# Kernel tuning notes

Measured on AMD Instinct MI355X. Metric: run time of the kernel, lower is better.

Reference implementation:

```python
import jax, jax.numpy as jnp
import numpy as np

N = 50000   # nodes
E = 800000  # edges
IN, H, O, C = 128, 256, 256, 64
G = 64      # graphs in batch


def setup_inputs() -> dict:
    key = jax.random.key(0)
    ks = jax.random.split(key, 10)
    x = jax.random.normal(ks[0], (N, IN), dtype=jnp.float32)
    edge_index = jax.random.randint(ks[1], (2, E), 0, N, dtype=jnp.int32)
    batch = jnp.sort(jax.random.randint(ks[2], (N,), 0, G, dtype=jnp.int32))
    # learned params (PyG GCNConv: weight [in, out] + bias [out]; nn.Linear)
    W1 = jax.random.normal(ks[3], (IN, H), dtype=jnp.float32) / np.sqrt(IN)
    b1 = jnp.zeros((H,), dtype=jnp.float32)
    W2 = jax.random.normal(ks[4], (H, O), dtype=jnp.float32) / np.sqrt(H)
    b2 = jnp.zeros((O,), dtype=jnp.float32)
    Wfc = jax.random.normal(ks[5], (O, C), dtype=jnp.float32) / np.sqrt(O)
    bfc = jnp.zeros((C,), dtype=jnp.float32)
    return {"x": x, "edge_index": edge_index, "batch": batch,
            "W1": W1, "b1": b1, "W2": W2, "b2": b2, "Wfc": Wfc, "bfc": bfc}


def reference(x, edge_index, batch, W1, b1, W2, b2, Wfc, bfc):
    src, dst = edge_index[0], edge_index[1]
    # degree with self-loops (PyG GCNConv default: add_self_loops=True, sym norm)
    deg = jax.ops.segment_sum(jnp.ones((E,), x.dtype), dst, num_segments=N) + 1.0
    dinv = jax.lax.rsqrt(deg)                      # D^{-1/2}
    edge_norm = (dinv[src] * dinv[dst])[:, None]   # [E, 1]
    self_norm = (dinv * dinv)[:, None]             # [N, 1] self-loop weight

    def gcn_conv(h, W, b):
        h = h @ W                                  # transform first (PyG order)
        agg = jax.ops.segment_sum(h[src] * edge_norm, dst, num_segments=N)
        return agg + h * self_norm + b

    h = jax.nn.gelu(gcn_conv(x, W1, b1), approximate=False)  # nn.GELU exact
    h = gcn_conv(h, W2, b2)

    # global_mean_pool over graph ids
    cnt = jax.ops.segment_sum(jnp.ones((N,), h.dtype), batch, num_segments=G)
    pooled = jax.ops.segment_sum(h, batch, num_segments=G) / jnp.maximum(cnt, 1.0)[:, None]
    return pooled @ Wfc + bfc                      # [G, C]
```

## Files before the change

kernel.cpp:

```cpp
#include <hip/hip_runtime.h>
#include <hip/hip_bf16.h>
#include <hip/hip_fp16.h>
#include <math.h>

#define NNODES 50000
#define NEDGES 800000
#define FIN 128
#define FH 256
#define NG 64
#define NC 64
#define NP 50176
#define QSK 196
#define SPLITX_ITEMS (NNODES * FIN / 4)
#define SPLITX_BLOCKS ((SPLITX_ITEMS + 255) / 256)
#define W1T_BLOCKS (FIN * 256 / 256)
#define GEMM_MB ((NNODES + 127) / 128)
#define GEMM_BLKS (GEMM_MB * 2)
#define QTR (NP / 4)

#define NBUCK 196
#define BCAP 5120
#define BIN_CHUNK 2048
#define BIN_BLOCKS ((NEDGES + BIN_CHUNK - 1) / BIN_CHUNK)

typedef unsigned short bhalf;
typedef __attribute__((ext_vector_type(8))) short bf16x8;
typedef __attribute__((ext_vector_type(4))) float f32x4;
typedef __attribute__((ext_vector_type(4))) unsigned short u16x4;

__device__ inline bhalf f2bf_rn(float f) {
    unsigned int u = __float_as_uint(f);
    u += 0x7FFFu + ((u >> 16) & 1u);
    return (bhalf)(u >> 16);
}
__device__ inline float bf2f(bhalf h) { return __uint_as_float(((unsigned int)h) << 16); }
__device__ inline float2 bfpair(unsigned int u) {
    return make_float2(__uint_as_float(u << 16), __uint_as_float(u & 0xFFFF0000u));
}


__global__ void splitx_kernel(const float* __restrict__ x, bhalf* __restrict__ xb,
                              const float* __restrict__ W1, bhalf* __restrict__ w1t,
                              int* __restrict__ bcur) {
    int b = blockIdx.x;
    if (b < SPLITX_BLOCKS) {
        int i = b * 256 + threadIdx.x;
        if (i < SPLITX_ITEMS) {
            float4 v = *reinterpret_cast<const float4*>(&x[i * 4]);
            u16x4 o = {f2bf_rn(v.x), f2bf_rn(v.y), f2bf_rn(v.z), f2bf_rn(v.w)};
            *reinterpret_cast<u16x4*>(&xb[i * 4]) = o;
        }
    } else if (b < SPLITX_BLOCKS + W1T_BLOCKS) {
        int i = (b - SPLITX_BLOCKS) * 256 + threadIdx.x;
        int k = i >> 8, n = i & 255;
        w1t[n * FIN + k] = f2bf_rn(W1[i]);
    } else {
        if (threadIdx.x < NBUCK) bcur[threadIdx.x] = threadIdx.x * BCAP;
    }
}


__global__ __launch_bounds__(256)
void bin_kernel(const int* __restrict__ src, const int* __restrict__ dst,
                int* __restrict__ bcur, unsigned int* __restrict__ binned) {
    __shared__ int hist[NBUCK];
    __shared__ int base[NBUCK];
    __shared__ int gb[NBUCK];
    __shared__ int lcur[NBUCK];
    __shared__ int scan_tmp[256];
    __shared__ unsigned int stage[BIN_CHUNK];
    __shared__ unsigned char bid[BIN_CHUNK];
    int t = threadIdx.x;
    int e0 = blockIdx.x * BIN_CHUNK;
    for (int i = t; i < NBUCK; i += 256) hist[i] = 0;
    __syncthreads();
#pragma unroll
    for (int k = 0; k < BIN_CHUNK / 256; k++) {
        int e = e0 + k * 256 + t;
        if (e < NEDGES) atomicAdd(&hist[dst[e] >> 8], 1);
    }
    __syncthreads();
    int v = (t < NBUCK) ? hist[t] : 0;
    scan_tmp[t] = v;
    __syncthreads();
#pragma unroll
    for (int off = 1; off < 256; off <<= 1) {
        int x = (t >= off) ? scan_tmp[t - off] : 0;
        __syncthreads();
        scan_tmp[t] += x;
        __syncthreads();
    }
    if (t < NBUCK) {
        int ex = scan_tmp[t] - v;
        base[t] = ex;
        lcur[t] = ex;
        gb[t] = (v > 0) ? atomicAdd(&bcur[t], v) : 0;
    }
    __syncthreads();
#pragma unroll
    for (int k = 0; k < BIN_CHUNK / 256; k++) {
        int e = e0 + k * 256 + t;
        if (e < NEDGES) {
            int s = src[e], d = dst[e];
            int b = d >> 8;
            int lp = atomicAdd(&lcur[b], 1);
            stage[lp] = (unsigned int)s | ((unsigned int)(d & 255) << 16);
            bid[lp] = (unsigned char)b;
        }
    }
    __syncthreads();
    int total = base[NBUCK - 1] + hist[NBUCK - 1];
    for (int i = t; i < total; i += 256) {
        int b = bid[i];
        binned[(size_t)gb[b] + (i - base[b])] = stage[i];
    }
}


__global__ __launch_bounds__(256)
void place_kernel(const unsigned int* __restrict__ binned, const int* __restrict__ bcur,
                  int* __restrict__ row_start, float* __restrict__ dinv,
                  unsigned int* __restrict__ edata) {
    __shared__ unsigned int stage[BCAP];
    __shared__ int sc[256];
    __shared__ int deg[256];
    __shared__ int lex[256];
    __shared__ int lcur[256];
    __shared__ unsigned short dih[256];
    __shared__ int s_ebase, s_cnt;
    int b = blockIdx.x, t = threadIdx.x;
    int c = (t < NBUCK) ? (bcur[t] - t * BCAP) : 0;
    sc[t] = c;
    __syncthreads();
#pragma unroll
    for (int off = 1; off < 256; off <<= 1) {
        int x = (t >= off) ? sc[t - off] : 0;
        __syncthreads();
        sc[t] += x;
        __syncthreads();
    }
    if (t == b) { s_ebase = sc[t] - c; s_cnt = c; }
    deg[t] = 0;
    __syncthreads();
    int cnt = s_cnt, eb = s_ebase;
    const unsigned int* bp = &binned[(size_t)b * BCAP];
    for (int i = t; i < cnt; i += 256) stage[i] = bp[i];
    __syncthreads();
    for (int i = t; i < cnt; i += 256) atomicAdd(&deg[(stage[i] >> 16) & 255], 1);
    __syncthreads();
    int d = deg[t];
    float di = rsqrtf((float)d + 1.0f);
    int gn = (b << 8) + t;
    if (gn < NNODES) dinv[gn] = di;
    dih[t] = __half_as_ushort(__float2half(di));
    sc[t] = d;
    __syncthreads();
#pragma unroll
    for (int off = 1; off < 256; off <<= 1) {
        int x = (t >= off) ? sc[t - off] : 0;
        __syncthreads();
        sc[t] += x;
        __syncthreads();
    }
    int lexv = sc[t] - d;
    lex[t] = lexv;
    lcur[t] = 0;
    if (gn <= NNODES) row_start[gn] = eb + lexv;
    __syncthreads();
    for (int i = t; i < cnt; i += 256) {
        unsigned int e = stage[i];
        int dl = (e >> 16) & 255;
        int pos = eb + lex[dl] + atomicAdd(&lcur[dl], 1);
        edata[pos] = (e & 0xFFFFu) | ((unsigned int)dih[dl] << 16);
    }
}


__global__ __launch_bounds__(256)
void gather128_kernel(const bhalf* __restrict__ xb, const unsigned int* __restrict__ edata,
                      const int* __restrict__ row_start, const float* __restrict__ dinv,
                      bhalf* __restrict__ z, int Nn) {
    int node = blockIdx.x * 4 + (threadIdx.x >> 6);
    if (node >= Nn) return;
    int lane = threadIdx.x & 63;
    int st = row_start[node];
    int cnt = row_start[node + 1] - st;
    float ax = 0.0f, ay = 0.0f;
    int j = 0;
    for (; j + 3 < cnt; j += 4) {
        unsigned int e0 = edata[st + j],     e1 = edata[st + j + 1];
        unsigned int e2 = edata[st + j + 2], e3 = edata[st + j + 3];
        int s0 = e0 & 0xFFFFu, s1 = e1 & 0xFFFFu, s2 = e2 & 0xFFFFu, s3 = e3 & 0xFFFFu;
        float2 v0 = bfpair(*reinterpret_cast<const unsigned int*>(&xb[(size_t)s0 * FIN + lane * 2]));
        float2 v1 = bfpair(*reinterpret_cast<const unsigned int*>(&xb[(size_t)s1 * FIN + lane * 2]));
        float2 v2 = bfpair(*reinterpret_cast<const unsigned int*>(&xb[(size_t)s2 * FIN + lane * 2]));
        float2 v3 = bfpair(*reinterpret_cast<const unsigned int*>(&xb[(size_t)s3 * FIN + lane * 2]));
        float n0 = dinv[s0], n1 = dinv[s1], n2 = dinv[s2], n3 = dinv[s3];
        ax += v0.x * n0 + v1.x * n1 + v2.x * n2 + v3.x * n3;
        ay += v0.y * n0 + v1.y * n1 + v2.y * n2 + v3.y * n3;
    }
    for (; j < cnt; j++) {
        unsigned int e0 = edata[st + j];
        int s0 = e0 & 0xFFFFu;
        float2 v0 = bfpair(*reinterpret_cast<const unsigned int*>(&xb[(size_t)s0 * FIN + lane * 2]));
        float n0 = dinv[s0];
        ax += v0.x * n0; ay += v0.y * n0;
    }
    float dn = dinv[node];
    float2 xv = bfpair(*reinterpret_cast<const unsigned int*>(&xb[(size_t)node * FIN + lane * 2]));
    ushort2 o = {f2bf_rn(dn * (ax + xv.x * dn)), f2bf_rn(dn * (ay + xv.y * dn))};
    *reinterpret_cast<ushort2*>(&z[(size_t)node * FIN + lane * 2]) = o;
}


__global__ __launch_bounds__(256)
void wt_build_kernel(const unsigned int* __restrict__ edata, const int* __restrict__ row_start,
                     const int* __restrict__ batch, const float* __restrict__ dinv,
                     bhalf* __restrict__ wthi, bhalf* __restrict__ wtlo) {
    __shared__ float acc[QTR];
    int g = blockIdx.x >> 2;
    int q = blockIdx.x & 3;
    int base = q * QTR;
    for (int i = threadIdx.x; i < QTR; i += 256) acc[i] = 0.0f;
    int lo = 0, hi = NNODES;
    while (lo < hi) { int m = (lo + hi) >> 1; if (batch[m] < g) lo = m + 1; else hi = m; }
    int na = lo;
    hi = NNODES;
    while (lo < hi) { int m = (lo + hi) >> 1; if (batch[m] < g + 1) lo = m + 1; else hi = m; }
    int nb = lo;
    int pa = row_start[na];
    int pb = row_start[nb];
    __syncthreads();
    for (int p = pa + threadIdx.x; p < pb; p += 256) {
        unsigned int e = edata[p];
        int s = (int)(e & 0xFFFFu) - base;
        if ((unsigned int)s < (unsigned int)QTR)
            atomicAdd(&acc[s], __half2float(__ushort_as_half((unsigned short)(e >> 16))));
    }
    __syncthreads();
    size_t rowo = (size_t)g * NP + base;
    for (int i = threadIdx.x; i < QTR; i += 256) {
        int s = base + i;
        float dv = (s < NNODES) ? dinv[s] : 0.0f;
        float v = acc[i];
        if (s >= na && s < nb) v += dv;
        v *= dv;
        bhalf hb = f2bf_rn(v);
        wthi[rowo + i] = hb;
        wtlo[rowo + i] = f2bf_rn(v - bf2f(hb));
    }
}


__global__ __launch_bounds__(256)
void gemm_kernel(const bhalf* __restrict__ A, const bhalf* __restrict__ Bt,
                 const float* __restrict__ bias, bhalf* __restrict__ h1t, int M, int Kp) {
    __shared__ bhalf As[128 * 72];
    __shared__ bhalf Bs[128 * 72];
    const int tid  = threadIdx.x;
    const int lane = tid & 63;
    const int wave = tid >> 6;
    const int quad = lane >> 4;
    const int l15  = lane & 15;
    const int wm = (wave & 1) * 64;
    const int wn = (wave >> 1) * 64;
    const int bm = (blockIdx.x >> 1) * 128;
    const int bn = (blockIdx.x & 1) * 128;

    f32x4 acc[4][4] = {};

    for (int k0 = 0; k0 < Kp; k0 += 64) {
#pragma unroll
        for (int i = 0; i < 4; i++) {
            int chunk = tid + i * 256;
            int r = chunk >> 3, c16 = chunk & 7;
            int gm = bm + r;
            float4 va = make_float4(0.f, 0.f, 0.f, 0.f);
            if (gm < M) va = *reinterpret_cast<const float4*>(&A[(size_t)gm * Kp + k0 + c16 * 8]);
            *reinterpret_cast<float4*>(&As[r * 72 + c16 * 8]) = va;
            float4 vb = *reinterpret_cast<const float4*>(&Bt[(size_t)(bn + r) * Kp + k0 + c16 * 8]);
            *reinterpret_cast<float4*>(&Bs[r * 72 + c16 * 8]) = vb;
        }
        __syncthreads();
#pragma unroll
        for (int kk = 0; kk < 64; kk += 32) {
            bf16x8 af[4], bfr[4];
#pragma unroll
            for (int mi = 0; mi < 4; mi++)
                af[mi] = *reinterpret_cast<const bf16x8*>(&As[(wm + mi * 16 + l15) * 72 + kk + quad * 8]);
#pragma unroll
            for (int ni = 0; ni < 4; ni++)
                bfr[ni] = *reinterpret_cast<const bf16x8*>(&Bs[(wn + ni * 16 + l15) * 72 + kk + quad * 8]);
#pragma unroll
            for (int mi = 0; mi < 4; mi++)
#pragma unroll
                for (int ni = 0; ni < 4; ni++)
                    acc[mi][ni] = __builtin_amdgcn_mfma_f32_16x16x32_bf16(af[mi], bfr[ni], acc[mi][ni], 0, 0, 0);
        }
        __syncthreads();
    }

#pragma unroll
    for (int mi = 0; mi < 4; mi++) {
        int row0 = bm + wm + mi * 16 + quad * 4;
#pragma unroll
        for (int ni = 0; ni < 4; ni++) {
            int col = bn + wn + ni * 16 + l15;
            float bv = bias[col];
            u16x4 o;
#pragma unroll
            for (int r = 0; r < 4; r++) {
                float v = acc[mi][ni][r] + bv;
                v = 0.5f * v * (1.0f + erff(v * 0.70710678118654752f));
                o[r] = f2bf_rn(v);
            }
            *reinterpret_cast<u16x4*>(&h1t[(size_t)col * NP + row0]) = o;
        }
    }
}


__global__ __launch_bounds__(256)
void qsum_mfma_kernel(const bhalf* __restrict__ h1t, const bhalf* __restrict__ wthi,
                      const bhalf* __restrict__ wtlo, float* __restrict__ qpart) {
    const int tid  = threadIdx.x;
    const int lane = tid & 63;
    const int wave = tid >> 6;
    const int quad = lane >> 4;
    const int l15  = lane & 15;
    const int m0 = wave * 64;
    const size_t kbase = (size_t)blockIdx.x * 256 + quad * 8;
    f32x4 acc[4][4] = {};
#pragma unroll
    for (int ks = 0; ks < 8; ks++) {
        size_t k0 = kbase + ks * 32;
        bf16x8 af[4], bh[4], bl[4];
#pragma unroll
        for (int mi = 0; mi < 4; mi++)
            af[mi] = *reinterpret_cast<const bf16x8*>(&h1t[(size_t)(m0 + mi * 16 + l15) * NP + k0]);
#pragma unroll
        for (int ni = 0; ni < 4; ni++) {
            bh[ni] = *reinterpret_cast<const bf16x8*>(&wthi[(size_t)(ni * 16 + l15) * NP + k0]);
            bl[ni] = *reinterpret_cast<const bf16x8*>(&wtlo[(size_t)(ni * 16 + l15) * NP + k0]);
        }
#pragma unroll
        for (int mi = 0; mi < 4; mi++)
#pragma unroll
            for (int ni = 0; ni < 4; ni++) {
                acc[mi][ni] = __builtin_amdgcn_mfma_f32_16x16x32_bf16(af[mi], bh[ni], acc[mi][ni], 0, 0, 0);
                acc[mi][ni] = __builtin_amdgcn_mfma_f32_16x16x32_bf16(af[mi], bl[ni], acc[mi][ni], 0, 0, 0);
            }
    }
    float* qp = &qpart[(size_t)blockIdx.x * NG * FH];
#pragma unroll
    for (int mi = 0; mi < 4; mi++) {
        int row0 = m0 + mi * 16 + quad * 4;
#pragma unroll
        for (int ni = 0; ni < 4; ni++) {
            int col = ni * 16 + l15;
            f32x4 o = {acc[mi][ni][0], acc[mi][ni][1], acc[mi][ni][2], acc[mi][ni][3]};
            *reinterpret_cast<f32x4*>(&qp[(size_t)col * FH + row0]) = o;
        }
    }
}


__global__ __launch_bounds__(256)
void p2fc_kernel(const float* __restrict__ qpart, const float* __restrict__ W2,
                 const float* __restrict__ b2, const int* __restrict__ batch,
                 const float* __restrict__ Wfc, const float* __restrict__ bfc,
                 float* __restrict__ out) {
    __shared__ float qg[FH];
    __shared__ float ps[FH];
    int g = blockIdx.x;
    int t = threadIdx.x;
    float s = 0.0f;
    for (int b = 0; b < QSK; b++)
        s += qpart[(size_t)b * NG * FH + (size_t)g * FH + t];
    qg[t] = s;
    int lo = 0, hi = NNODES;
    while (lo < hi) { int m = (lo + hi) >> 1; if (batch[m] < g) lo = m + 1; else hi = m; }
    int a = lo;
    lo = 0; hi = NNODES;
    while (lo < hi) { int m = (lo + hi) >> 1; if (batch[m] < g + 1) lo = m + 1; else hi = m; }
    float inv = 1.0f / fmaxf((float)(lo - a), 1.0f);
    __syncthreads();
    float acc = 0.0f;
    for (int k = 0; k < FH; k++)
        acc += qg[k] * W2[k * FH + t];
    ps[t] = acc * inv + b2[t];
    __syncthreads();
    if (t < NC) {
        float a2 = 0.0f;
        for (int cc = 0; cc < FH; cc++)
            a2 += ps[cc] * Wfc[cc * NC + t];
        out[g * NC + t] = a2 + bfc[t];
    }
}


extern "C" void kernel_launch(void* const* d_in, const int* in_sizes, int n_in,
                              void* d_out, int out_size, void* d_ws, size_t ws_size,
                              hipStream_t stream) {
    const float* x    = (const float*)d_in[0];
    const int*   ei   = (const int*)d_in[1];
    const int*   batch= (const int*)d_in[2];
    const float* W1   = (const float*)d_in[3];
    const float* b1   = (const float*)d_in[4];
    const float* W2   = (const float*)d_in[5];
    const float* b2   = (const float*)d_in[6];
    const float* Wfc  = (const float*)d_in[7];
    const float* bfc  = (const float*)d_in[8];
    float* out = (float*)d_out;

    const int* src = ei;
    const int* dst = ei + NEDGES;

    bhalf* xb        = (bhalf*)d_ws;
    bhalf* zb        = xb + (size_t)NNODES * FIN;
    bhalf* h1t       = zb + (size_t)NNODES * FIN;
    unsigned int* edata  = (unsigned int*)(h1t + (size_t)FH * NP);
    unsigned int* binned = edata + NEDGES;
    int*   row_start = (int*)(binned + (size_t)NBUCK * BCAP);
    int*   bcur      = row_start + NNODES + 256;
    float* dinv      = (float*)(bcur + 256);
    bhalf* w1t       = (bhalf*)(dinv + NNODES + 256);
    bhalf* wthi      = w1t + 256 * FIN;
    bhalf* wtlo      = wthi + (size_t)NG * NP;
    float* qpart     = (float*)(wtlo + (size_t)NG * NP);

    splitx_kernel<<<SPLITX_BLOCKS + W1T_BLOCKS + 1, 256, 0, stream>>>(x, xb, W1, w1t, bcur);
    bin_kernel<<<BIN_BLOCKS, 256, 0, stream>>>(src, dst, bcur, binned);
    place_kernel<<<NBUCK, 256, 0, stream>>>(binned, bcur, row_start, dinv, edata);

    gather128_kernel<<<(NNODES + 3) / 4, 256, 0, stream>>>(xb, edata, row_start, dinv,
                                                           zb, NNODES);
    wt_build_kernel<<<NG * 4, 256, 0, stream>>>(edata, row_start, batch, dinv, wthi, wtlo);
    gemm_kernel<<<GEMM_BLKS, 256, 0, stream>>>(zb, w1t, b1, h1t, NNODES, FIN);

    qsum_mfma_kernel<<<QSK, 256, 0, stream>>>(h1t, wthi, wtlo, qpart);
    p2fc_kernel<<<NG, FH, 0, stream>>>(qpart, W2, b2, batch, Wfc, bfc, out);
}
```

Before: 246.8 us.

## Fuse GEMM epilogue with pooled-weight reduction and merge binning with conversion

The layer-1 GEMM now keeps its GELU output tile in shared memory and multiplies it right away against the per-graph weight rows (hi/lo bf16) with MFMA. This removes the h1t round trip through global memory and the separate qsum kernel. The binning, x-to-bf16 conversion and W1 transpose now run in a single launch, with bucket counters reset by a memset instead of the old init block. The cost is more partial buffers (one per GEMM block) for p2fc to reduce, plus extra shared-memory reuse inside the GEMM.

```diff
diff --git a/kernel.cpp b/kernel.cpp
--- a/kernel.cpp
+++ b/kernel.cpp
@@ -10,7 +10,6 @@
 #define NG 64
 #define NC 64
 #define NP 50176
-#define QSK 196
 #define SPLITX_ITEMS (NNODES * FIN / 4)
 #define SPLITX_BLOCKS ((SPLITX_ITEMS + 255) / 256)
 #define W1T_BLOCKS (FIN * 256 / 256)
@@ -22,6 +21,7 @@
 #define BCAP 5120
 #define BIN_CHUNK 2048
 #define BIN_BLOCKS ((NEDGES + BIN_CHUNK - 1) / BIN_CHUNK)
+#define K1_BLOCKS (BIN_BLOCKS + SPLITX_BLOCKS + W1T_BLOCKS)
 
 typedef unsigned short bhalf;
 typedef __attribute__((ext_vector_type(8))) short bf16x8;
@@ -39,30 +39,27 @@
 }
 
 
-__global__ void splitx_kernel(const float* __restrict__ x, bhalf* __restrict__ xb,
-                              const float* __restrict__ W1, bhalf* __restrict__ w1t,
-                              int* __restrict__ bcur) {
-    int b = blockIdx.x;
-    if (b < SPLITX_BLOCKS) {
-        int i = b * 256 + threadIdx.x;
-        if (i < SPLITX_ITEMS) {
-            float4 v = *reinterpret_cast<const float4*>(&x[i * 4]);
-            u16x4 o = {f2bf_rn(v.x), f2bf_rn(v.y), f2bf_rn(v.z), f2bf_rn(v.w)};
-            *reinterpret_cast<u16x4*>(&xb[i * 4]) = o;
-        }
-    } else if (b < SPLITX_BLOCKS + W1T_BLOCKS) {
-        int i = (b - SPLITX_BLOCKS) * 256 + threadIdx.x;
-        int k = i >> 8, n = i & 255;
-        w1t[n * FIN + k] = f2bf_rn(W1[i]);
-    } else {
-        if (threadIdx.x < NBUCK) bcur[threadIdx.x] = threadIdx.x * BCAP;
-    }
-}
-
-
-__global__ __launch_bounds__(256)
-void bin_kernel(const int* __restrict__ src, const int* __restrict__ dst,
-                int* __restrict__ bcur, unsigned int* __restrict__ binned) {
+__global__ __launch_bounds__(256)
+void k1_kernel(const int* __restrict__ src, const int* __restrict__ dst,
+               int* __restrict__ bcur, unsigned int* __restrict__ binned,
+               const float* __restrict__ x, bhalf* __restrict__ xb,
+               const float* __restrict__ W1, bhalf* __restrict__ w1t) {
+    if (blockIdx.x >= BIN_BLOCKS) {
+        int b = blockIdx.x - BIN_BLOCKS;
+        if (b < SPLITX_BLOCKS) {
+            int i = b * 256 + threadIdx.x;
+            if (i < SPLITX_ITEMS) {
+                float4 v = *reinterpret_cast<const float4*>(&x[i * 4]);
+                u16x4 o = {f2bf_rn(v.x), f2bf_rn(v.y), f2bf_rn(v.z), f2bf_rn(v.w)};
+                *reinterpret_cast<u16x4*>(&xb[i * 4]) = o;
+            }
+        } else {
+            int i = (b - SPLITX_BLOCKS) * 256 + threadIdx.x;
+            int k = i >> 8, n = i & 255;
+            w1t[n * FIN + k] = f2bf_rn(W1[i]);
+        }
+        return;
+    }
     __shared__ int hist[NBUCK];
     __shared__ int base[NBUCK];
     __shared__ int gb[NBUCK];
@@ -85,9 +82,9 @@
     __syncthreads();
 #pragma unroll
     for (int off = 1; off < 256; off <<= 1) {
-        int x = (t >= off) ? scan_tmp[t - off] : 0;
-        __syncthreads();
-        scan_tmp[t] += x;
+        int xx = (t >= off) ? scan_tmp[t - off] : 0;
+        __syncthreads();
+        scan_tmp[t] += xx;
         __syncthreads();
     }
     if (t < NBUCK) {
@@ -112,7 +109,7 @@
     int total = base[NBUCK - 1] + hist[NBUCK - 1];
     for (int i = t; i < total; i += 256) {
         int b = bid[i];
-        binned[(size_t)gb[b] + (i - base[b])] = stage[i];
+        binned[(size_t)b * BCAP + gb[b] + (i - base[b])] = stage[i];
     }
 }
 
@@ -129,7 +126,7 @@
     __shared__ unsigned short dih[256];
     __shared__ int s_ebase, s_cnt;
     int b = blockIdx.x, t = threadIdx.x;
-    int c = (t < NBUCK) ? (bcur[t] - t * BCAP) : 0;
+    int c = (t < NBUCK) ? bcur[t] : 0;
     sc[t] = c;
     __syncthreads();
 #pragma unroll
@@ -253,10 +250,12 @@
 
 
 __global__ __launch_bounds__(256)
-void gemm_kernel(const bhalf* __restrict__ A, const bhalf* __restrict__ Bt,
-                 const float* __restrict__ bias, bhalf* __restrict__ h1t, int M, int Kp) {
-    __shared__ bhalf As[128 * 72];
-    __shared__ bhalf Bs[128 * 72];
+void gemmq_kernel(const bhalf* __restrict__ A, const bhalf* __restrict__ Bt,
+                  const float* __restrict__ bias, const bhalf* __restrict__ wthi,
+                  const bhalf* __restrict__ wtlo, float* __restrict__ qpart, int M) {
+    __shared__ alignas(16) bhalf smem[2 * 128 * 72];
+    bhalf* As = smem;
+    bhalf* Bs = smem + 128 * 72;
     const int tid  = threadIdx.x;
     const int lane = tid & 63;
     const int wave = tid >> 6;
@@ -269,16 +268,16 @@
 
     f32x4 acc[4][4] = {};
 
-    for (int k0 = 0; k0 < Kp; k0 += 64) {
+    for (int k0 = 0; k0 < FIN; k0 += 64) {
 #pragma unroll
         for (int i = 0; i < 4; i++) {
             int chunk = tid + i * 256;
             int r = chunk >> 3, c16 = chunk & 7;
             int gm = bm + r;
             float4 va = make_float4(0.f, 0.f, 0.f, 0.f);
-            if (gm < M) va = *reinterpret_cast<const float4*>(&A[(size_t)gm * Kp + k0 + c16 * 8]);
+            if (gm < M) va = *reinterpret_cast<const float4*>(&A[(size_t)gm * FIN + k0 + c16 * 8]);
             *reinterpret_cast<float4*>(&As[r * 72 + c16 * 8]) = va;
-            float4 vb = *reinterpret_cast<const float4*>(&Bt[(size_t)(bn + r) * Kp + k0 + c16 * 8]);
+            float4 vb = *reinterpret_cast<const float4*>(&Bt[(size_t)(bn + r) * FIN + k0 + c16 * 8]);
             *reinterpret_cast<float4*>(&Bs[r * 72 + c16 * 8]) = vb;
         }
         __syncthreads();
@@ -300,13 +299,14 @@
         __syncthreads();
     }
 
+    bhalf* h1s = smem;
 #pragma unroll
     for (int mi = 0; mi < 4; mi++) {
-        int row0 = bm + wm + mi * 16 + quad * 4;
+        int node0 = wm + mi * 16 + quad * 4;
 #pragma unroll
         for (int ni = 0; ni < 4; ni++) {
-            int col = bn + wn + ni * 16 + l15;
-            float bv = bias[col];
+            int col = wn + ni * 16 + l15;
+            float bv = bias[bn + col];
             u16x4 o;
 #pragma unroll
             for (int r = 0; r < 4; r++) {
@@ -314,52 +314,40 @@
                 v = 0.5f * v * (1.0f + erff(v * 0.70710678118654752f));
                 o[r] = f2bf_rn(v);
             }
-            *reinterpret_cast<u16x4*>(&h1t[(size_t)col * NP + row0]) = o;
-        }
-    }
-}
-
-
-__global__ __launch_bounds__(256)
-void qsum_mfma_kernel(const bhalf* __restrict__ h1t, const bhalf* __restrict__ wthi,
-                      const bhalf* __restrict__ wtlo, float* __restrict__ qpart) {
-    const int tid  = threadIdx.x;
-    const int lane = tid & 63;
-    const int wave = tid >> 6;
-    const int quad = lane >> 4;
-    const int l15  = lane & 15;
-    const int m0 = wave * 64;
-    const size_t kbase = (size_t)blockIdx.x * 256 + quad * 8;
-    f32x4 acc[4][4] = {};
-#pragma unroll
-    for (int ks = 0; ks < 8; ks++) {
-        size_t k0 = kbase + ks * 32;
-        bf16x8 af[4], bh[4], bl[4];
-#pragma unroll
-        for (int mi = 0; mi < 4; mi++)
-            af[mi] = *reinterpret_cast<const bf16x8*>(&h1t[(size_t)(m0 + mi * 16 + l15) * NP + k0]);
-#pragma unroll
-        for (int ni = 0; ni < 4; ni++) {
-            bh[ni] = *reinterpret_cast<const bf16x8*>(&wthi[(size_t)(ni * 16 + l15) * NP + k0]);
-            bl[ni] = *reinterpret_cast<const bf16x8*>(&wtlo[(size_t)(ni * 16 + l15) * NP + k0]);
-        }
-#pragma unroll
-        for (int mi = 0; mi < 4; mi++)
-#pragma unroll
-            for (int ni = 0; ni < 4; ni++) {
-                acc[mi][ni] = __builtin_amdgcn_mfma_f32_16x16x32_bf16(af[mi], bh[ni], acc[mi][ni], 0, 0, 0);
-                acc[mi][ni] = __builtin_amdgcn_mfma_f32_16x16x32_bf16(af[mi], bl[ni], acc[mi][ni], 0, 0, 0);
+            *reinterpret_cast<u16x4*>(&h1s[col * 136 + node0]) = o;
+        }
+    }
+    __syncthreads();
+
+    f32x4 qacc[4][2] = {};
+    const int c0 = wave * 32;
+#pragma unroll
+    for (int kk2 = 0; kk2 < 128; kk2 += 32) {
+        bf16x8 bfr[2];
+#pragma unroll
+        for (int ct = 0; ct < 2; ct++)
+            bfr[ct] = *reinterpret_cast<const bf16x8*>(&h1s[(c0 + ct * 16 + l15) * 136 + kk2 + quad * 8]);
+        size_t nodeg = (size_t)(bm + kk2 + quad * 8);
+#pragma unroll
+        for (int gt = 0; gt < 4; gt++) {
+            bf16x8 afh = *reinterpret_cast<const bf16x8*>(&wthi[(size_t)(gt * 16 + l15) * NP + nodeg]);
+            bf16x8 afl = *reinterpret_cast<const bf16x8*>(&wtlo[(size_t)(gt * 16 + l15) * NP + nodeg]);
+#pragma unroll
+            for (int ct = 0; ct < 2; ct++) {
+                qacc[gt][ct] = __builtin_amdgcn_mfma_f32_16x16x32_bf16(afh, bfr[ct], qacc[gt][ct], 0, 0, 0);
+                qacc[gt][ct] = __builtin_amdgcn_mfma_f32_16x16x32_bf16(afl, bfr[ct], qacc[gt][ct], 0, 0, 0);
             }
-    }
-    float* qp = &qpart[(size_t)blockIdx.x * NG * FH];
-#pragma unroll
-    for (int mi = 0; mi < 4; mi++) {
-        int row0 = m0 + mi * 16 + quad * 4;
-#pragma unroll
-        for (int ni = 0; ni < 4; ni++) {
-            int col = ni * 16 + l15;
-            f32x4 o = {acc[mi][ni][0], acc[mi][ni][1], acc[mi][ni][2], acc[mi][ni][3]};
-            *reinterpret_cast<f32x4*>(&qp[(size_t)col * FH + row0]) = o;
+        }
+    }
+    float* qp = &qpart[(size_t)blockIdx.x * NG * 128];
+#pragma unroll
+    for (int gt = 0; gt < 4; gt++) {
+#pragma unroll
+        for (int ct = 0; ct < 2; ct++) {
+            int col = c0 + ct * 16 + l15;
+#pragma unroll
+            for (int r = 0; r < 4; r++)
+                qp[(gt * 16 + quad * 4 + r) * 128 + col] = qacc[gt][ct][r];
         }
     }
 }
@@ -374,10 +362,11 @@
     __shared__ float ps[FH];
     int g = blockIdx.x;
     int t = threadIdx.x;
+    int half = t >> 7, kc = t & 127;
     float s = 0.0f;
-    for (int b = 0; b < QSK; b++)
-        s += qpart[(size_t)b * NG * FH + (size_t)g * FH + t];
-    qg[t] = s;
+    for (int m = 0; m < GEMM_MB; m++)
+        s += qpart[(size_t)(m * 2 + half) * NG * 128 + (size_t)g * 128 + kc];
+    qg[half * 128 + kc] = s;
     int lo = 0, hi = NNODES;
     while (lo < hi) { int m = (lo + hi) >> 1; if (batch[m] < g) lo = m + 1; else hi = m; }
     int a = lo;
@@ -418,8 +407,7 @@
 
     bhalf* xb        = (bhalf*)d_ws;
     bhalf* zb        = xb + (size_t)NNODES * FIN;
-    bhalf* h1t       = zb + (size_t)NNODES * FIN;
-    unsigned int* edata  = (unsigned int*)(h1t + (size_t)FH * NP);
+    unsigned int* edata  = (unsigned int*)(zb + (size_t)NNODES * FIN);
     unsigned int* binned = edata + NEDGES;
     int*   row_start = (int*)(binned + (size_t)NBUCK * BCAP);
     int*   bcur      = row_start + NNODES + 256;
@@ -429,15 +417,16 @@
     bhalf* wtlo      = wthi + (size_t)NG * NP;
     float* qpart     = (float*)(wtlo + (size_t)NG * NP);
 
-    splitx_kernel<<<SPLITX_BLOCKS + W1T_BLOCKS + 1, 256, 0, stream>>>(x, xb, W1, w1t, bcur);
-    bin_kernel<<<BIN_BLOCKS, 256, 0, stream>>>(src, dst, bcur, binned);
+    (void)hipMemsetAsync(bcur, 0, NBUCK * 4, stream);
+
+    k1_kernel<<<K1_BLOCKS, 256, 0, stream>>>(src, dst, bcur, binned, x, xb, W1, w1t);
     place_kernel<<<NBUCK, 256, 0, stream>>>(binned, bcur, row_start, dinv, edata);
 
     gather128_kernel<<<(NNODES + 3) / 4, 256, 0, stream>>>(xb, edata, row_start, dinv,
                                                            zb, NNODES);
     wt_build_kernel<<<NG * 4, 256, 0, stream>>>(edata, row_start, batch, dinv, wthi, wtlo);
-    gemm_kernel<<<GEMM_BLKS, 256, 0, stream>>>(zb, w1t, b1, h1t, NNODES, FIN);
-
-    qsum_mfma_kernel<<<QSK, 256, 0, stream>>>(h1t, wthi, wtlo, qpart);
+
+    gemmq_kernel<<<GEMM_BLKS, 256, 0, stream>>>(zb, w1t, b1, wthi, wtlo, qpart, NNODES);
+
     p2fc_kernel<<<NG, FH, 0, stream>>>(qpart, W2, b2, batch, Wfc, bfc, out);
 }
```

After: 247.9 us. No clear change (+0.4%).
